# Kernel tuning notes

Hardware: AMD Instinct MI355X
Metric: run time of the kernel (lower is better)

## Reference

```python
import jax, jax.numpy as jnp
import numpy as np

B, C, H, W, K = 32, 192, 64, 64, 32
CLAMP = 1.5

def setup_inputs() -> dict:
    key = jax.random.key(0)
    ks = jax.random.split(key, 6)
    return {
        "x": jax.random.normal(ks[0], (B, C, H, W), dtype=jnp.float32),
        "a": jax.random.normal(ks[1], (C,), dtype=jnp.float32),
        "b": jax.random.normal(ks[2], (C,), dtype=jnp.float32),
        "alpha": jax.random.normal(ks[3], (C, K), dtype=jnp.float32),
        "id_gain": jax.random.normal(ks[4], (C,), dtype=jnp.float32),
        "bias": jax.random.normal(ks[5], (C,), dtype=jnp.float32),
    }

def _cubic_basis(t):
    t2 = t * t
    t3 = t2 * t
    b0 = (1.0 - 3.0 * t + 3.0 * t2 - t3) / 6.0
    b1 = (4.0 - 6.0 * t2 + 3.0 * t3) / 6.0
    b2 = (1.0 + 3.0 * t + 3.0 * t2 - 3.0 * t3) / 6.0
    b3 = t3 / 6.0
    return b0, b1, b2, b3

def reference(x, a, b, alpha, id_gain, bias):
    Kk = alpha.shape[-1]
    c = x.shape[1]
    x_aff = x * a[None, :, None, None] + b[None, :, None, None]
    x_aff = jnp.clip(x_aff, -CLAMP, CLAMP)
    # map [-1, 1] -> [0, K-1]
    u = (x_aff + 1.0) * 0.5 * (Kk - 1)
    i = jnp.floor(u).astype(jnp.int32)
    t = jnp.clip(u - i.astype(u.dtype), 0.0, 1.0)
    i0 = jnp.clip(i - 1, 0, Kk - 1)
    i1 = jnp.clip(i, 0, Kk - 1)
    i2 = jnp.clip(i + 1, 0, Kk - 1)
    i3 = jnp.clip(i + 2, 0, Kk - 1)
    b0, b1, b2, b3 = _cubic_basis(t)
    cidx = jnp.arange(c)[None, :, None, None]  # broadcasts with [B,C,H,W] idx
    a0 = alpha[cidx, i0]
    a1 = alpha[cidx, i1]
    a2 = alpha[cidx, i2]
    a3 = alpha[cidx, i3]
    spline = a0 * b0 + a1 * b1 + a2 * b2 + a3 * b3
    return id_gain[None, :, None, None] * x + spline + bias[None, :, None, None]
```

## Files before the change

kernel.cpp:

```cpp
#include <hip/hip_runtime.h>


#define TOTAL_ELEMS 25165824
#define TOTAL4      6291456
#define PLANE4      1024
#define NCH         192
#define BLOCKS      2048
#define TPB         256

__device__ __forceinline__ float kan_elem(float xx, float a_c, float b_c,
                                          float g_c, float s_c, float av) {
    float xa = fmaf(xx, a_c, b_c);
    xa = fminf(fmaxf(xa, -1.5f), 1.5f);
    float u  = (xa + 1.0f) * 15.5f;
    float fi = floorf(u);
    int   i  = (int)fi;
    float t  = u - fi;
    int i0 = min(max(i - 1, 0), 31);
    int i1 = min(max(i,     0), 31);
    int i2 = min(max(i + 1, 0), 31);
    int i3 = min(max(i + 2, 0), 31);
    float a0 = __shfl(av, i0, 64);
    float a1 = __shfl(av, i1, 64);
    float a2 = __shfl(av, i2, 64);
    float a3 = __shfl(av, i3, 64);
    float t2 = t * t, t3 = t2 * t;
    const float k6 = 1.0f / 6.0f;
    float w0 = (1.0f - 3.0f*t + 3.0f*t2 -      t3) * k6;
    float w1 = (4.0f -           6.0f*t2 + 3.0f*t3) * k6;
    float w2 = (1.0f + 3.0f*t + 3.0f*t2 - 3.0f*t3) * k6;
    float w3 = t3 * k6;
    float spline = a0*w0 + a1*w1 + a2*w2 + a3*w3;
    return fmaf(g_c, xx, spline + s_c);
}

__global__ __launch_bounds__(TPB) void kan_cubic_kernel(
    const float* __restrict__ x, const float* __restrict__ a,
    const float* __restrict__ b, const float* __restrict__ alpha,
    const float* __restrict__ id_gain, const float* __restrict__ bias,
    float* __restrict__ out)
{
    const int j = threadIdx.x & 31;
    int g = blockIdx.x * TPB + threadIdx.x;
    #pragma unroll 1
    for (; g < TOTAL4; g += BLOCKS * TPB) {
        int c = (g >> 10) % NCH;
        c = __builtin_amdgcn_readfirstlane(c);
        float a_c = a[c];
        float b_c = b[c];
        float g_c = id_gain[c];
        float s_c = bias[c];
        float av  = alpha[(c << 5) + j];

        float4 xv = reinterpret_cast<const float4*>(x)[g];
        float4 ov;
        ov.x = kan_elem(xv.x, a_c, b_c, g_c, s_c, av);
        ov.y = kan_elem(xv.y, a_c, b_c, g_c, s_c, av);
        ov.z = kan_elem(xv.z, a_c, b_c, g_c, s_c, av);
        ov.w = kan_elem(xv.w, a_c, b_c, g_c, s_c, av);
        reinterpret_cast<float4*>(out)[g] = ov;
    }
}

extern "C" void kernel_launch(void* const* d_in, const int* in_sizes, int n_in,
                              void* d_out, int out_size, void* d_ws, size_t ws_size,
                              hipStream_t stream) {
    const float* x       = (const float*)d_in[0];
    const float* a       = (const float*)d_in[1];
    const float* b       = (const float*)d_in[2];
    const float* alpha   = (const float*)d_in[3];
    const float* id_gain = (const float*)d_in[4];
    const float* bias    = (const float*)d_in[5];
    float* out = (float*)d_out;
    kan_cubic_kernel<<<BLOCKS, TPB, 0, stream>>>(x, a, b, alpha, id_gain, bias, out);
}
```

Measured before the change: 186.2 us.

## Fully unroll grid-stride loop with prefetch, hoisted per-channel params, nontemporal stores

Replaces the grid-stride loop with a fully unrolled 12-iteration schedule. It relies on the channel of each of the 12 strided chunks cycling through three fixed offsets (0, +128, +64 mod 192), so all per-channel parameters and alpha rows are loaded once up front. The next three float4 loads are issued before computing the current three, and outputs use nontemporal stores. The cubic B-spline weights are also rewritten in a cheaper fma form. This hardcodes the problem size and adds register pressure.

New measurement: 186.9 us. About the same (+0.4%).

```diff
diff --git a/kernel.cpp b/kernel.cpp
--- a/kernel.cpp
+++ b/kernel.cpp
@@ -1,18 +1,19 @@
 #include <hip/hip_runtime.h>
 
 
-#define TOTAL_ELEMS 25165824
-#define TOTAL4      6291456
-#define PLANE4      1024
-#define NCH         192
-#define BLOCKS      2048
-#define TPB         256
+#define NCH     192
+#define TOTAL4  6291456
+#define BLOCKS  2048
+#define TPB     256
+#define STRIDE  (BLOCKS * TPB)
+
+typedef float f32x4 __attribute__((ext_vector_type(4)));
 
 __device__ __forceinline__ float kan_elem(float xx, float a_c, float b_c,
                                           float g_c, float s_c, float av) {
     float xa = fmaf(xx, a_c, b_c);
     xa = fminf(fmaxf(xa, -1.5f), 1.5f);
-    float u  = (xa + 1.0f) * 15.5f;
+    float u  = fmaf(xa, 15.5f, 15.5f);
     float fi = floorf(u);
     int   i  = (int)fi;
     float t  = u - fi;
@@ -20,18 +21,29 @@
     int i1 = min(max(i,     0), 31);
     int i2 = min(max(i + 1, 0), 31);
     int i3 = min(max(i + 2, 0), 31);
-    float a0 = __shfl(av, i0, 64);
-    float a1 = __shfl(av, i1, 64);
-    float a2 = __shfl(av, i2, 64);
-    float a3 = __shfl(av, i3, 64);
-    float t2 = t * t, t3 = t2 * t;
+    float p0 = __shfl(av, i0, 64);
+    float p1 = __shfl(av, i1, 64);
+    float p2 = __shfl(av, i2, 64);
+    float p3 = __shfl(av, i3, 64);
+    float s  = 1.0f - t;
+    float t2 = t * t, s2 = s * s;
     const float k6 = 1.0f / 6.0f;
-    float w0 = (1.0f - 3.0f*t + 3.0f*t2 -      t3) * k6;
-    float w1 = (4.0f -           6.0f*t2 + 3.0f*t3) * k6;
-    float w2 = (1.0f + 3.0f*t + 3.0f*t2 - 3.0f*t3) * k6;
-    float w3 = t3 * k6;
-    float spline = a0*w0 + a1*w1 + a2*w2 + a3*w3;
+    float w0 = s2 * s * k6;
+    float w3 = t2 * t * k6;
+    float w1 = fmaf(t2, fmaf(t, 0.5f, -1.0f), 2.0f / 3.0f);
+    float w2 = fmaf(s2, fmaf(s, 0.5f, -1.0f), 2.0f / 3.0f);
+    float spline = fmaf(p0, w0, fmaf(p1, w1, fmaf(p2, w2, p3 * w3)));
     return fmaf(g_c, xx, spline + s_c);
+}
+
+__device__ __forceinline__ f32x4 kan4(f32x4 xv, float a_c, float b_c,
+                                      float g_c, float s_c, float av) {
+    f32x4 ov;
+    ov.x = kan_elem(xv.x, a_c, b_c, g_c, s_c, av);
+    ov.y = kan_elem(xv.y, a_c, b_c, g_c, s_c, av);
+    ov.z = kan_elem(xv.z, a_c, b_c, g_c, s_c, av);
+    ov.w = kan_elem(xv.w, a_c, b_c, g_c, s_c, av);
+    return ov;
 }
 
 __global__ __launch_bounds__(TPB) void kan_cubic_kernel(
@@ -40,25 +52,44 @@
     const float* __restrict__ id_gain, const float* __restrict__ bias,
     float* __restrict__ out)
 {
-    const int j = threadIdx.x & 31;
-    int g = blockIdx.x * TPB + threadIdx.x;
-    #pragma unroll 1
-    for (; g < TOTAL4; g += BLOCKS * TPB) {
-        int c = (g >> 10) % NCH;
-        c = __builtin_amdgcn_readfirstlane(c);
-        float a_c = a[c];
-        float b_c = b[c];
-        float g_c = id_gain[c];
-        float s_c = bias[c];
-        float av  = alpha[(c << 5) + j];
+    const int j  = threadIdx.x & 31;
+    const int g0 = blockIdx.x * TPB + threadIdx.x;
 
-        float4 xv = reinterpret_cast<const float4*>(x)[g];
-        float4 ov;
-        ov.x = kan_elem(xv.x, a_c, b_c, g_c, s_c, av);
-        ov.y = kan_elem(xv.y, a_c, b_c, g_c, s_c, av);
-        ov.z = kan_elem(xv.z, a_c, b_c, g_c, s_c, av);
-        ov.w = kan_elem(xv.w, a_c, b_c, g_c, s_c, av);
-        reinterpret_cast<float4*>(out)[g] = ov;
+    int c0 = __builtin_amdgcn_readfirstlane((g0 >> 10) % NCH);
+    int c1 = c0 + 128; if (c1 >= NCH) c1 -= NCH;
+    int c2 = c0 + 64;  if (c2 >= NCH) c2 -= NCH;
+
+    float a0c = a[c0], b0c = b[c0], g0c = id_gain[c0], s0c = bias[c0];
+    float a1c = a[c1], b1c = b[c1], g1c = id_gain[c1], s1c = bias[c1];
+    float a2c = a[c2], b2c = b[c2], g2c = id_gain[c2], s2c = bias[c2];
+    float av0 = alpha[(c0 << 5) + j];
+    float av1 = alpha[(c1 << 5) + j];
+    float av2 = alpha[(c2 << 5) + j];
+
+    const f32x4* __restrict__ x4 = reinterpret_cast<const f32x4*>(x);
+    f32x4* __restrict__ o4 = reinterpret_cast<f32x4*>(out);
+
+    f32x4 v0 = x4[g0 + 0 * STRIDE];
+    f32x4 v1 = x4[g0 + 1 * STRIDE];
+    f32x4 v2 = x4[g0 + 2 * STRIDE];
+
+    #pragma unroll
+    for (int bb = 0; bb < 4; ++bb) {
+        f32x4 n0, n1, n2;
+        if (bb < 3) {
+            n0 = x4[g0 + (3 * bb + 3) * STRIDE];
+            n1 = x4[g0 + (3 * bb + 4) * STRIDE];
+            n2 = x4[g0 + (3 * bb + 5) * STRIDE];
+        } else {
+            n0 = v0; n1 = v1; n2 = v2;
+        }
+        f32x4 r0 = kan4(v0, a0c, b0c, g0c, s0c, av0);
+        f32x4 r1 = kan4(v1, a1c, b1c, g1c, s1c, av1);
+        f32x4 r2 = kan4(v2, a2c, b2c, g2c, s2c, av2);
+        __builtin_nontemporal_store(r0, &o4[g0 + (3 * bb + 0) * STRIDE]);
+        __builtin_nontemporal_store(r1, &o4[g0 + (3 * bb + 1) * STRIDE]);
+        __builtin_nontemporal_store(r2, &o4[g0 + (3 * bb + 2) * STRIDE]);
+        v0 = n0; v1 = n1; v2 = n2;
     }
 }
 
```
